# Kernel tuning notes

Measured on AMD Instinct MI355X. Metric: run time of the kernel, lower is better.

The kernel has to match this reference:

```python
import jax, jax.numpy as jnp
import numpy as np

COMMITMENT_COST = 0.25
LAMBDA_KL = 1.0
EPS = 1e-10


def setup_inputs() -> dict:
    key = jax.random.key(0)
    k1, k2 = jax.random.split(key)
    x = jax.random.normal(k1, (8, 4096, 256), dtype=jnp.float32)
    embedding = jax.random.normal(k2, (1024, 256), dtype=jnp.float32)
    return {"x": x, "embedding": embedding}


def reference(x, embedding):
    B, T, D = x.shape
    M, _ = embedding.shape
    x_sg = jax.lax.stop_gradient(x)
    x_flat = x_sg.reshape(-1, D)  # [N, D]
    distances = (jnp.sum(embedding ** 2, axis=1)[None, :]
                 + jnp.sum(x_flat ** 2, axis=1, keepdims=True)
                 - 2.0 * (x_flat @ embedding.T))  # [N, M]
    indices = jnp.argmin(distances.astype(jnp.float32), axis=-1)  # [N]
    quantized = embedding[indices].reshape(B, T, D)
    # losses (x detached in both terms, matching torch)
    loss = (COMMITMENT_COST * jnp.mean((x_sg - quantized) ** 2)
            + jnp.mean((quantized - x_sg) ** 2)) * LAMBDA_KL
    # straight-through estimator
    quantized_st = x + jax.lax.stop_gradient(quantized - x)
    # avg of one-hot encodings == normalized code counts (avoids NxM one-hot)
    N = B * T
    counts = jnp.zeros((M,), dtype=jnp.float32).at[indices].add(1.0)
    avg_probs = counts / N
    perplexity = jnp.exp(-jnp.sum(avg_probs * jnp.log(avg_probs + EPS)))
    return (quantized_st, loss, indices.reshape(B, T), perplexity)
```

## Files before the change

kernel.cpp:

```cpp
#include <hip/hip_runtime.h>


constexpr int D = 256;
constexpr int M = 1024;
constexpr int ROWS = 128;

typedef _Float16 f16;
typedef __attribute__((ext_vector_type(8))) _Float16 f16x8;
typedef __attribute__((ext_vector_type(4))) float f32x4;

constexpr size_t WS_ENORM_F = 1028;
constexpr size_t WS_TAB_B   = 8320;
constexpr size_t WS_NEEDED  = 1056896;

__device__ inline void gload_lds16(const void* g, void* l) {
    __builtin_amdgcn_global_load_lds(
        (const __attribute__((address_space(1))) unsigned int*)(g),
        (__attribute__((address_space(3))) unsigned int*)(l), 16, 0, 0);
}

__global__ __launch_bounds__(256) void prep_kernel(const float* __restrict__ e,
                                                   float* __restrict__ ws) {
    const int b = blockIdx.x, t = threadIdx.x;
    if (b < 256) {
        int v    = b * 256 + t;
        int lane = v & 63, unit = v >> 6;
        int spl = unit & 1, kk = (unit >> 1) & 7, t16 = unit >> 4;
        int lr = lane & 15, q = lane >> 4;
        const float* p = e + (size_t)(t16 * 16 + lr) * D + kk * 32 + q * 8;
        f32x4 a = *reinterpret_cast<const f32x4*>(p);
        f32x4 c = *reinterpret_cast<const f32x4*>(p + 4);
        f16 h0=(f16)a.x,h1=(f16)a.y,h2=(f16)a.z,h3=(f16)a.w;
        f16 h4=(f16)c.x,h5=(f16)c.y,h6=(f16)c.z,h7=(f16)c.w;
        f16x8 out;
        if (spl == 0) out = (f16x8){h0,h1,h2,h3,h4,h5,h6,h7};
        else          out = (f16x8){(f16)(a.x-(float)h0),(f16)(a.y-(float)h1),
                                    (f16)(a.z-(float)h2),(f16)(a.w-(float)h3),
                                    (f16)(c.x-(float)h4),(f16)(c.y-(float)h5),
                                    (f16)(c.z-(float)h6),(f16)(c.w-(float)h7)};
        *reinterpret_cast<f16x8*>((char*)ws + WS_TAB_B + (size_t)v * 16) = out;
    } else {
        int row  = (b - 256) * 4 + (t >> 6);
        int lane = t & 63;
        f32x4 a = *reinterpret_cast<const f32x4*>(e + (size_t)row * D + lane * 4);
        float s = fmaf(a.x, a.x, fmaf(a.y, a.y, fmaf(a.z, a.z, a.w * a.w)));
#pragma unroll
        for (int o = 32; o > 0; o >>= 1) s += __shfl_down(s, o, 64);
        if (lane == 0) ws[WS_ENORM_F + row] = s;
    }
}

__global__ __launch_bounds__(512, 2) void vq_fused_kernel(
    const float* __restrict__ x, const float* __restrict__ e,
    float* __restrict__ outQ, float* __restrict__ outIdx, float* __restrict__ ws)
{
    __shared__ ushort ebuf[2][2][8192];
    __shared__ float  en_s[M];
    __shared__ float  mval[ROWS];
    __shared__ int    midx[ROWS];
    __shared__ int    fidx[ROWS];
    __shared__ float  lsum[8];

    const int tid  = threadIdx.x;
    const int w    = __builtin_amdgcn_readfirstlane(tid >> 6);
    const int l    = tid & 63;
    const int lr   = l & 15, q = l >> 4;
    const int team = w >> 2;
    const int wr   = w & 3;
    const int R    = blockIdx.x * ROWS;
    const char* tab = (const char*)ws + WS_TAB_B;

    auto stage = [&](int buf, int g) {
#pragma unroll
        for (int i = 0; i < 4; ++i) {
            int S = w * 4 + i, tm = S >> 4, sg = S & 15;
            gload_lds16(tab + (size_t)(tm * 32 + g) * 16384 + sg * 1024 + l * 16,
                        &ebuf[buf][tm][sg * 512]);
        }
    };
    stage(0, 0);

    if (tid < 256) {
        f32x4 v = *reinterpret_cast<const f32x4*>(ws + WS_ENORM_F + tid * 4);
        *reinterpret_cast<f32x4*>(&en_s[tid * 4]) = v;
    }

    f16x8 Xh[2][8], Xl[2][8];
    float xn[2];
#pragma unroll
    for (int cf = 0; cf < 2; ++cf) {
        float s = 0.f;
#pragma unroll
        for (int kk = 0; kk < 8; ++kk) {
            const float* p = x + (size_t)(R + wr * 32 + cf * 16 + lr) * D + kk * 32 + q * 8;
            f32x4 a = *reinterpret_cast<const f32x4*>(p);
            f32x4 c = *reinterpret_cast<const f32x4*>(p + 4);
            f16 h0=(f16)a.x,h1=(f16)a.y,h2=(f16)a.z,h3=(f16)a.w;
            f16 h4=(f16)c.x,h5=(f16)c.y,h6=(f16)c.z,h7=(f16)c.w;
            Xh[cf][kk] = (f16x8){h0,h1,h2,h3,h4,h5,h6,h7};
            Xl[cf][kk] = (f16x8){(f16)(a.x-(float)h0),(f16)(a.y-(float)h1),
                                 (f16)(a.z-(float)h2),(f16)(a.w-(float)h3),
                                 (f16)(c.x-(float)h4),(f16)(c.y-(float)h5),
                                 (f16)(c.z-(float)h6),(f16)(c.w-(float)h7)};
            s = fmaf(a.x,a.x,fmaf(a.y,a.y,fmaf(a.z,a.z,fmaf(a.w,a.w,
                fmaf(c.x,c.x,fmaf(c.y,c.y,fmaf(c.z,c.z,fmaf(c.w,c.w,s))))))));
        }
        s += __shfl_xor(s, 16, 64);
        s += __shfl_xor(s, 32, 64);
        xn[cf] = s;
    }
    __syncthreads();

    float bV[2] = {3.4e38f, 3.4e38f};
    int   bI[2] = {0, 0};

    for (int g = 0; g < 32; ++g) {
        const ushort* eb = &ebuf[g & 1][team][0];
        if (g < 31) stage((g + 1) & 1, g + 1);

        f32x4 accA[2], accB[2];
#pragma unroll
        for (int cf = 0; cf < 2; ++cf) {
            accA[cf] = (f32x4){0.f,0.f,0.f,0.f};
            accB[cf] = (f32x4){0.f,0.f,0.f,0.f};
        }
        __builtin_amdgcn_s_setprio(1);
#pragma unroll
        for (int kk = 0; kk < 8; ++kk) {
            f16x8 Ah = *reinterpret_cast<const f16x8*>(eb + (kk*2+0)*512 + l*8);
            f16x8 Al = *reinterpret_cast<const f16x8*>(eb + (kk*2+1)*512 + l*8);
            accA[0] = __builtin_amdgcn_mfma_f32_16x16x32_f16(Ah, Xh[0][kk], accA[0], 0, 0, 0);
            accA[0] = __builtin_amdgcn_mfma_f32_16x16x32_f16(Ah, Xl[0][kk], accA[0], 0, 0, 0);
            accB[0] = __builtin_amdgcn_mfma_f32_16x16x32_f16(Al, Xh[0][kk], accB[0], 0, 0, 0);
            accA[1] = __builtin_amdgcn_mfma_f32_16x16x32_f16(Ah, Xh[1][kk], accA[1], 0, 0, 0);
            accA[1] = __builtin_amdgcn_mfma_f32_16x16x32_f16(Ah, Xl[1][kk], accA[1], 0, 0, 0);
            accB[1] = __builtin_amdgcn_mfma_f32_16x16x32_f16(Al, Xh[1][kk], accB[1], 0, 0, 0);
        }
        __builtin_amdgcn_s_setprio(0);
        __syncthreads();

        const int mbase = team * 512 + g * 16;
        f32x4 en4 = *reinterpret_cast<const f32x4*>(&en_s[mbase + q * 4]);
#pragma unroll
        for (int i = 0; i < 4; ++i) {
            int mi = mbase + q * 4 + i;
#pragma unroll
            for (int cf = 0; cf < 2; ++cf) {
                float dv = fmaf(-2.f, accA[cf][i] + accB[cf][i], en4[i]);
                if (dv < bV[cf]) { bV[cf] = dv; bI[cf] = mi; }
            }
        }
    }

#pragma unroll
    for (int cf = 0; cf < 2; ++cf) {
#pragma unroll
        for (int mk = 16; mk <= 32; mk <<= 1) {
            float ov = __shfl_xor(bV[cf], mk, 64);
            int   oi = __shfl_xor(bI[cf], mk, 64);
            if (ov < bV[cf] || (ov == bV[cf] && oi < bI[cf])) { bV[cf] = ov; bI[cf] = oi; }
        }
    }
    if (team == 0 && q == 0) {
#pragma unroll
        for (int cf = 0; cf < 2; ++cf) {
            int r = wr * 32 + cf * 16 + lr;
            mval[r] = bV[cf]; midx[r] = bI[cf];
        }
    }
    __syncthreads();
    if (team == 1 && q == 0) {
        float ls = 0.f;
#pragma unroll
        for (int cf = 0; cf < 2; ++cf) {
            int r = wr * 32 + cf * 16 + lr;
            float av = mval[r]; int ai = midx[r];
            float fv; int fi;
            if (bV[cf] < av) { fv = bV[cf]; fi = bI[cf]; } else { fv = av; fi = ai; }
            fidx[r] = fi;
            outIdx[R + r] = (float)fi;
            atomicAdd(ws + 1 + fi, 1.0f);
            ls += fv + xn[cf];
        }
#pragma unroll
        for (int o = 8; o > 0; o >>= 1) ls += __shfl_down(ls, o, 16);
        if (lr == 0) lsum[w] = ls;
    }
    __syncthreads();
    if (tid == 0) atomicAdd(ws, lsum[4] + lsum[5] + lsum[6] + lsum[7]);

#pragma unroll
    for (int it = 0; it < 16; ++it) {
        int u = it * 512 + tid;
        int row = u >> 6, c4 = u & 63;
        f32x4 v = *reinterpret_cast<const f32x4*>(e + (size_t)fidx[row] * D + c4 * 4);
        __builtin_nontemporal_store(v, reinterpret_cast<f32x4*>(outQ + (size_t)(R + row) * D + c4 * 4));
    }
}

__global__ void enorm_kernel(const float* __restrict__ e, float* __restrict__ enorm) {
    int m = blockIdx.x, l = threadIdx.x;
    const f32x4 v = *reinterpret_cast<const f32x4*>(e + m * D + l * 4);
    float s = fmaf(v.x, v.x, fmaf(v.y, v.y, fmaf(v.z, v.z, v.w * v.w)));
#pragma unroll
    for (int o = 32; o > 0; o >>= 1) s += __shfl_down(s, o, 64);
    if (l == 0) enorm[m] = s;
}

__global__ __launch_bounds__(256, 2) void vq_main_kernel(
    const float* __restrict__ x, const float* __restrict__ e,
    float* __restrict__ outQ, float* __restrict__ outIdx, float* __restrict__ ws) {
    __shared__ f32x4 xs[64][64];
    __shared__ float cval[4][64];
    __shared__ int   cidx[4][64];
    __shared__ int   fidx[64];
    const int tid = threadIdx.x, row0 = blockIdx.x * 64;
#pragma unroll
    for (int it = 0; it < 16; ++it) {
        int f = it * 256 + tid, rr = f >> 6, c4 = f & 63;
        xs[rr][c4 ^ (rr & 7)] = *reinterpret_cast<const f32x4*>(x + (row0 + rr) * D + c4 * 4);
    }
    __syncthreads();
    const int r = tid & 63, c = __builtin_amdgcn_readfirstlane(tid >> 6), sw = r & 7;
    float xnorm = 0.f;
    if (c == 0) {
        f32x4 a = (f32x4){0.f,0.f,0.f,0.f};
        for (int d4 = 0; d4 < 64; ++d4) {
            f32x4 xv = xs[r][d4 ^ sw];
            a.x = fmaf(xv.x, xv.x, a.x); a.y = fmaf(xv.y, xv.y, a.y);
            a.z = fmaf(xv.z, xv.z, a.z); a.w = fmaf(xv.w, xv.w, a.w);
        }
        xnorm = (a.x + a.y) + (a.z + a.w);
    }
    const float* __restrict__ enorm = ws + WS_ENORM_F;
    float bestVal = 3.4e38f; int bestIdx = 0;
    for (int chunk = 0; chunk < M / 32; ++chunk) {
        const int m0 = chunk * 32 + c * 8;
        f32x4 acc[8];
#pragma unroll
        for (int mi = 0; mi < 8; ++mi) acc[mi] = (f32x4){0.f,0.f,0.f,0.f};
#pragma unroll 2
        for (int d4 = 0; d4 < 64; ++d4) {
            const f32x4 xv = xs[r][d4 ^ sw];
#pragma unroll
            for (int mi = 0; mi < 8; ++mi) {
                const f32x4 ev = *reinterpret_cast<const f32x4*>(e + (m0 + mi) * D + d4 * 4);
                acc[mi].x = fmaf(xv.x, ev.x, acc[mi].x); acc[mi].y = fmaf(xv.y, ev.y, acc[mi].y);
                acc[mi].z = fmaf(xv.z, ev.z, acc[mi].z); acc[mi].w = fmaf(xv.w, ev.w, acc[mi].w);
            }
        }
#pragma unroll
        for (int mi = 0; mi < 8; ++mi) {
            float dot = (acc[mi].x + acc[mi].y) + (acc[mi].z + acc[mi].w);
            float val = enorm[m0 + mi] - 2.0f * dot;
            if (val < bestVal) { bestVal = val; bestIdx = m0 + mi; }
        }
    }
    cval[c][r] = bestVal; cidx[c][r] = bestIdx;
    __syncthreads();
    if (c == 0) {
        float bv = bestVal; int bi = bestIdx;
#pragma unroll
        for (int cc = 1; cc < 4; ++cc) {
            float v = cval[cc][r]; int i = cidx[cc][r];
            if (v < bv || (v == bv && i < bi)) { bv = v; bi = i; }
        }
        fidx[r] = bi; outIdx[row0 + r] = (float)bi;
        atomicAdd(ws + 1 + bi, 1.0f);
        float dist = bv + xnorm;
#pragma unroll
        for (int o = 32; o > 0; o >>= 1) dist += __shfl_down(dist, o, 64);
        if (r == 0) atomicAdd(ws, dist);
    }
    __syncthreads();
#pragma unroll
    for (int it = 0; it < 16; ++it) {
        int f = it * 256 + tid, rr = f >> 6, c4 = f & 63;
        *reinterpret_cast<f32x4*>(outQ + (row0 + rr) * D + c4 * 4) =
            *reinterpret_cast<const f32x4*>(e + fidx[rr] * D + c4 * 4);
    }
}

__global__ void vq_final_kernel(const float* __restrict__ ws,
                                float* __restrict__ outLoss, float* __restrict__ outPpl,
                                float invN, float invND) {
    int t = threadIdx.x;
    float p = ws[1 + t] * invN;
    float term = p * logf(p + 1e-10f);
#pragma unroll
    for (int o = 32; o > 0; o >>= 1) term += __shfl_down(term, o, 64);
    __shared__ float s[16];
    if ((t & 63) == 0) s[t >> 6] = term;
    __syncthreads();
    if (t == 0) {
        float tot = 0.f;
#pragma unroll
        for (int i = 0; i < 16; ++i) tot += s[i];
        *outPpl  = expf(-tot);
        *outLoss = 1.25f * ws[0] * invND;
    }
}

extern "C" void kernel_launch(void* const* d_in, const int* in_sizes, int n_in,
                              void* d_out, int out_size, void* d_ws, size_t ws_size,
                              hipStream_t stream) {
    const float* x = (const float*)d_in[0];
    const float* e = (const float*)d_in[1];
    const int NX = in_sizes[0];
    const int N  = NX / D;

    float* out     = (float*)d_out;
    float* outQ    = out;
    float* outLoss = out + NX;
    float* outIdx  = out + NX + 1;
    float* outPpl  = out + NX + 1 + N;
    float* ws      = (float*)d_ws;

    (void)hipMemsetAsync(d_ws, 0, 4100, stream);
    if (ws_size >= WS_NEEDED && (N % ROWS) == 0) {
        prep_kernel<<<512, 256, 0, stream>>>(e, ws);
        vq_fused_kernel<<<N / ROWS, 512, 0, stream>>>(x, e, outQ, outIdx, ws);
    } else {
        enorm_kernel<<<M, 64, 0, stream>>>(e, ws + WS_ENORM_F);
        vq_main_kernel<<<N / 64, 256, 0, stream>>>(x, e, outQ, outIdx, ws);
    }
    vq_final_kernel<<<1, 1024, 0, stream>>>(ws, outLoss, outPpl,
                                            1.0f / (float)N, 1.0f / (float)NX);
}
```

Baseline: 95.58 us.

## Shrink fused VQ block to 64 rows, 2 waves, no codebook split

The fused kernel drops from 512 threads over 128 rows, where two wave teams each scan half of the codebook and merge, to 128 threads over 64 rows, where each wave scans all 1024 codes. The cross-team argmin merge through shared memory is removed and the grid doubles in block count. The aim is better occupancy and load balance with less synchronisation. The cost is that each staged codebook tile now feeds only 64 rows, so codebook LDS traffic per row doubles, and the serial loop runs 64 iterations instead of 32.

New measurement: 111.2 us. 16.4% more time.

```diff
diff --git a/kernel.cpp b/kernel.cpp
--- a/kernel.cpp
+++ b/kernel.cpp
@@ -3,7 +3,7 @@
 
 constexpr int D = 256;
 constexpr int M = 1024;
-constexpr int ROWS = 128;
+constexpr int ROWS = 64;
 
 typedef _Float16 f16;
 typedef __attribute__((ext_vector_type(8))) _Float16 f16x8;
@@ -50,39 +50,37 @@
     }
 }
 
-__global__ __launch_bounds__(512, 2) void vq_fused_kernel(
+__global__ __launch_bounds__(128, 2) void vq_fused_kernel(
     const float* __restrict__ x, const float* __restrict__ e,
     float* __restrict__ outQ, float* __restrict__ outIdx, float* __restrict__ ws)
 {
-    __shared__ ushort ebuf[2][2][8192];
+    __shared__ ushort ebuf[2][8192];
     __shared__ float  en_s[M];
-    __shared__ float  mval[ROWS];
-    __shared__ int    midx[ROWS];
     __shared__ int    fidx[ROWS];
-    __shared__ float  lsum[8];
-
-    const int tid  = threadIdx.x;
-    const int w    = __builtin_amdgcn_readfirstlane(tid >> 6);
-    const int l    = tid & 63;
-    const int lr   = l & 15, q = l >> 4;
-    const int team = w >> 2;
-    const int wr   = w & 3;
-    const int R    = blockIdx.x * ROWS;
+    __shared__ float  lsum[2];
+
+    const int tid = threadIdx.x;
+    const int w   = __builtin_amdgcn_readfirstlane(tid >> 6);
+    const int l   = tid & 63;
+    const int lr  = l & 15, q = l >> 4;
+    const int R   = blockIdx.x * ROWS;
     const char* tab = (const char*)ws + WS_TAB_B;
 
     auto stage = [&](int buf, int g) {
 #pragma unroll
-        for (int i = 0; i < 4; ++i) {
-            int S = w * 4 + i, tm = S >> 4, sg = S & 15;
-            gload_lds16(tab + (size_t)(tm * 32 + g) * 16384 + sg * 1024 + l * 16,
-                        &ebuf[buf][tm][sg * 512]);
+        for (int i = 0; i < 8; ++i) {
+            int sg = w * 8 + i;
+            gload_lds16(tab + (size_t)g * 16384 + sg * 1024 + l * 16,
+                        &ebuf[buf][sg * 512]);
         }
     };
     stage(0, 0);
 
-    if (tid < 256) {
-        f32x4 v = *reinterpret_cast<const f32x4*>(ws + WS_ENORM_F + tid * 4);
-        *reinterpret_cast<f32x4*>(&en_s[tid * 4]) = v;
+    {
+        f32x4 v0 = *reinterpret_cast<const f32x4*>(ws + WS_ENORM_F + tid * 8);
+        f32x4 v1 = *reinterpret_cast<const f32x4*>(ws + WS_ENORM_F + tid * 8 + 4);
+        *reinterpret_cast<f32x4*>(&en_s[tid * 8])     = v0;
+        *reinterpret_cast<f32x4*>(&en_s[tid * 8 + 4]) = v1;
     }
 
     f16x8 Xh[2][8], Xl[2][8];
@@ -92,7 +90,7 @@
         float s = 0.f;
 #pragma unroll
         for (int kk = 0; kk < 8; ++kk) {
-            const float* p = x + (size_t)(R + wr * 32 + cf * 16 + lr) * D + kk * 32 + q * 8;
+            const float* p = x + (size_t)(R + w * 32 + cf * 16 + lr) * D + kk * 32 + q * 8;
             f32x4 a = *reinterpret_cast<const f32x4*>(p);
             f32x4 c = *reinterpret_cast<const f32x4*>(p + 4);
             f16 h0=(f16)a.x,h1=(f16)a.y,h2=(f16)a.z,h3=(f16)a.w;
@@ -114,9 +112,9 @@
     float bV[2] = {3.4e38f, 3.4e38f};
     int   bI[2] = {0, 0};
 
-    for (int g = 0; g < 32; ++g) {
-        const ushort* eb = &ebuf[g & 1][team][0];
-        if (g < 31) stage((g + 1) & 1, g + 1);
+    for (int g = 0; g < 64; ++g) {
+        const ushort* eb = &ebuf[g & 1][0];
+        if (g < 63) stage((g + 1) & 1, g + 1);
 
         f32x4 accA[2], accB[2];
 #pragma unroll
@@ -139,7 +137,7 @@
         __builtin_amdgcn_s_setprio(0);
         __syncthreads();
 
-        const int mbase = team * 512 + g * 16;
+        const int mbase = g * 16;
         f32x4 en4 = *reinterpret_cast<const f32x4*>(&en_s[mbase + q * 4]);
 #pragma unroll
         for (int i = 0; i < 4; ++i) {
@@ -161,37 +159,26 @@
             if (ov < bV[cf] || (ov == bV[cf] && oi < bI[cf])) { bV[cf] = ov; bI[cf] = oi; }
         }
     }
-    if (team == 0 && q == 0) {
+    if (q == 0) {
+        float ls = 0.f;
 #pragma unroll
         for (int cf = 0; cf < 2; ++cf) {
-            int r = wr * 32 + cf * 16 + lr;
-            mval[r] = bV[cf]; midx[r] = bI[cf];
-        }
-    }
-    __syncthreads();
-    if (team == 1 && q == 0) {
-        float ls = 0.f;
-#pragma unroll
-        for (int cf = 0; cf < 2; ++cf) {
-            int r = wr * 32 + cf * 16 + lr;
-            float av = mval[r]; int ai = midx[r];
-            float fv; int fi;
-            if (bV[cf] < av) { fv = bV[cf]; fi = bI[cf]; } else { fv = av; fi = ai; }
-            fidx[r] = fi;
-            outIdx[R + r] = (float)fi;
-            atomicAdd(ws + 1 + fi, 1.0f);
-            ls += fv + xn[cf];
+            int r = w * 32 + cf * 16 + lr;
+            fidx[r] = bI[cf];
+            outIdx[R + r] = (float)bI[cf];
+            atomicAdd(ws + 1 + bI[cf], 1.0f);
+            ls += bV[cf] + xn[cf];
         }
 #pragma unroll
         for (int o = 8; o > 0; o >>= 1) ls += __shfl_down(ls, o, 16);
         if (lr == 0) lsum[w] = ls;
     }
     __syncthreads();
-    if (tid == 0) atomicAdd(ws, lsum[4] + lsum[5] + lsum[6] + lsum[7]);
-
-#pragma unroll
-    for (int it = 0; it < 16; ++it) {
-        int u = it * 512 + tid;
+    if (tid == 0) atomicAdd(ws, lsum[0] + lsum[1]);
+
+#pragma unroll
+    for (int it = 0; it < 32; ++it) {
+        int u = it * 128 + tid;
         int row = u >> 6, c4 = u & 63;
         f32x4 v = *reinterpret_cast<const f32x4*>(e + (size_t)fidx[row] * D + c4 * 4);
         __builtin_nontemporal_store(v, reinterpret_cast<f32x4*>(outQ + (size_t)(R + row) * D + c4 * 4));
@@ -319,7 +306,7 @@
     (void)hipMemsetAsync(d_ws, 0, 4100, stream);
     if (ws_size >= WS_NEEDED && (N % ROWS) == 0) {
         prep_kernel<<<512, 256, 0, stream>>>(e, ws);
-        vq_fused_kernel<<<N / ROWS, 512, 0, stream>>>(x, e, outQ, outIdx, ws);
+        vq_fused_kernel<<<N / ROWS, 128, 0, stream>>>(x, e, outQ, outIdx, ws);
     } else {
         enorm_kernel<<<M, 64, 0, stream>>>(e, ws + WS_ENORM_F);
         vq_main_kernel<<<N / 64, 256, 0, stream>>>(x, e, outQ, outIdx, ws);
```
